# Kernel optimization log

Measured on AMD Instinct MI355X. Metric: run time of the kernel, lower is better.

## Reference

```python
import jax, jax.numpy as jnp
import numpy as np

DIM, NHEADS = 1024, 16
HD = DIM // NHEADS
ROPE_BASE = 10000.0


def rope_cos_sin(seq_len, hd):
    inv_freq = 1.0 / (ROPE_BASE ** (jnp.arange(0, hd, 2, dtype=jnp.float32) / hd))
    t = jnp.arange(seq_len, dtype=jnp.float32)
    freqs = jnp.outer(t, inv_freq)              # [N, hd/2]
    emb = jnp.concatenate([freqs, freqs], -1)   # [N, hd]
    return jnp.cos(emb), jnp.sin(emb)


def rotate_half(x):
    h = x.shape[-1] // 2
    return jnp.concatenate([-x[..., h:], x[..., :h]], -1)


def setup_inputs() -> dict:
    key = jax.random.key(0)
    ks = jax.random.split(key, 5)
    B, N = 1, 2048
    x = jax.random.normal(ks[0], (B, N, DIM), jnp.float32)
    wq = jax.random.normal(ks[1], (DIM, DIM), jnp.float32) * 0.02
    wk = jax.random.normal(ks[2], (DIM, DIM), jnp.float32) * 0.02
    wv = jax.random.normal(ks[3], (DIM, DIM), jnp.float32) * 0.02
    wp = jax.random.normal(ks[4], (DIM, DIM), jnp.float32) * 0.02
    return {"x": x, "wq": wq, "wk": wk, "wv": wv, "wp": wp}


def reference(x, wq, wk, wv, wp):
    B, N, D = x.shape
    H, hd = NHEADS, HD
    # nn.Linear: y = x @ W.T (weights stored [out, in])
    q = (x @ wq.T).reshape(B, N, H, hd)
    k = (x @ wk.T).reshape(B, N, H, hd)
    v = (x @ wv.T).reshape(B, N, H, hd)
    cos, sin = rope_cos_sin(N, hd)
    cos = cos[None, :, None, :]
    sin = sin[None, :, None, :]
    q = q * cos + rotate_half(q) * sin
    k = k * cos + rotate_half(k) * sin
    # SDPA (no mask, non-causal, eval -> no dropout)
    scale = 1.0 / jnp.sqrt(jnp.float32(hd))
    logits = jnp.einsum("bqhd,bkhd->bhqk", q, k) * scale
    attn = jax.nn.softmax(logits, axis=-1)
    out = jnp.einsum("bhqk,bkhd->bqhd", attn, v).reshape(B, N, D)
    return out @ wp.T
```

## Files before the change

### kernel.cpp

```cpp
#include <hip/hip_runtime.h>

typedef short s16x8 __attribute__((ext_vector_type(8)));
typedef float f32x4 __attribute__((ext_vector_type(4)));

__device__ __forceinline__ unsigned short f2bf(float f) {
    unsigned int u = __float_as_uint(f);
    u += 0x7fff + ((u >> 16) & 1);
    return (unsigned short)(u >> 16);
}
__device__ __forceinline__ float bf2f(unsigned short h) {
    return __uint_as_float(((unsigned int)h) << 16);
}
__device__ __forceinline__ f32x4 mfma16(s16x8 a, s16x8 b, f32x4 c) {
    return __builtin_amdgcn_mfma_f32_16x16x32_bf16(a, b, c, 0, 0, 0);
}
__device__ __forceinline__ void async16(const void* g, void* l) {
    __builtin_amdgcn_global_load_lds(
        (const __attribute__((address_space(1))) void*)g,
        (__attribute__((address_space(3))) void*)l, 16, 0, 0);
}

__global__ __launch_bounds__(256) void convert_all(
    const float* __restrict__ x,  const float* __restrict__ wq,
    const float* __restrict__ wk, const float* __restrict__ wv,
    const float* __restrict__ wp,
    unsigned short* __restrict__ xb, unsigned short* __restrict__ wqkvb,
    unsigned short* __restrict__ wpb)
{
    const size_t XN = 2048u * 1024u, WN = 1024u * 1024u;
    size_t e = ((size_t)blockIdx.x * 256 + threadIdx.x) * 4;
    const float* s; unsigned short* d;
    if (e < XN)                { s = x  + e;               d = xb    + e; }
    else if (e < XN + WN)      { s = wq + (e - XN);        d = wqkvb + (e - XN); }
    else if (e < XN + 2 * WN)  { s = wk + (e - XN - WN);   d = wqkvb + (e - XN); }
    else if (e < XN + 3 * WN)  { s = wv + (e - XN - 2*WN); d = wqkvb + (e - XN); }
    else                       { s = wp + (e - XN - 3*WN); d = wpb   + (e - XN - 3*WN); }
    float4 v = *(const float4*)s;
    ushort4 o;
    o.x = f2bf(v.x); o.y = f2bf(v.y); o.z = f2bf(v.z); o.w = f2bf(v.w);
    *(ushort4*)d = o;
}

template<int BN, int C32>
__global__ __launch_bounds__(256) void gemm_mfma(
    const unsigned short* __restrict__ A,
    const unsigned short* __restrict__ B,
    void* __restrict__ C, int Ntot)
{
    __shared__ unsigned short As[128 * 64];
    __shared__ unsigned short Bs[BN * 64];

    const int tid  = threadIdx.x;
    const int wave = tid >> 6, lane = tid & 63;
    const int l16  = lane & 15, quad = lane >> 4;
    const int m0   = blockIdx.y * 128, n0 = blockIdx.x * BN;
    const int wm   = (wave & 1) * 64, wn = (wave >> 1) * (BN / 2);
    constexpr int NT = BN / 32;

    const int srow = lane >> 3;
    const int scol = (lane & 7) * 8;

    f32x4 acc[4][NT] = {};

    for (int k0 = 0; k0 < 1024; k0 += 64) {
        #pragma unroll
        for (int i = 0; i < 4; i++) {
            int j = wave * 4 + i;
            async16(A + (size_t)(m0 + j * 8 + srow) * 1024 + k0 + scol, &As[j * 512]);
        }
        #pragma unroll
        for (int i = 0; i < BN / 32; i++) {
            int j = wave * (BN / 32) + i;
            async16(B + (size_t)(n0 + j * 8 + srow) * 1024 + k0 + scol, &Bs[j * 512]);
        }
        __syncthreads();

        #pragma unroll
        for (int ks = 0; ks < 2; ks++) {
            s16x8 af[4], bfr[NT];
            #pragma unroll
            for (int mt = 0; mt < 4; mt++)
                af[mt] = *(const s16x8*)&As[(wm + mt * 16 + l16) * 64 + ks * 32 + quad * 8];
            #pragma unroll
            for (int nt = 0; nt < NT; nt++)
                bfr[nt] = *(const s16x8*)&Bs[(wn + nt * 16 + l16) * 64 + ks * 32 + quad * 8];
            #pragma unroll
            for (int mt = 0; mt < 4; mt++)
                #pragma unroll
                for (int nt = 0; nt < NT; nt++)
                    acc[mt][nt] = mfma16(af[mt], bfr[nt], acc[mt][nt]);
        }
        __syncthreads();
    }

    #pragma unroll
    for (int mt = 0; mt < 4; mt++)
        #pragma unroll
        for (int nt = 0; nt < NT; nt++)
            #pragma unroll
            for (int r = 0; r < 4; r++) {
                int m = m0 + wm + mt * 16 + quad * 4 + r;
                int n = n0 + wn + nt * 16 + l16;
                size_t idx = (size_t)m * Ntot + n;
                if (C32) ((float*)C)[idx] = acc[mt][nt][r];
                else     ((unsigned short*)C)[idx] = f2bf(acc[mt][nt][r]);
            }
}

__global__ __launch_bounds__(256) void rope_kernel(unsigned short* __restrict__ qkv)
{
    int idx = blockIdx.x * 256 + threadIdx.x;
    int i = idx & 31;
    int h = (idx >> 5) & 15;
    int n = idx >> 9;
    float ang = (float)n * exp2f((float)i * (-13.287712379549449f / 32.0f));
    float c, s;
    sincosf(ang, &c, &s);
    size_t base = (size_t)n * 3072 + h * 64 + i;
    float a0 = bf2f(qkv[base]), a1 = bf2f(qkv[base + 32]);
    qkv[base]      = f2bf(a0 * c + a1 * s);
    qkv[base + 32] = f2bf(a1 * c - a0 * s);
    float b0 = bf2f(qkv[base + 1024]), b1 = bf2f(qkv[base + 1056]);
    qkv[base + 1024] = f2bf(b0 * c + b1 * s);
    qkv[base + 1056] = f2bf(b1 * c - b0 * s);
}

__global__ __launch_bounds__(256) void attn_kernel(
    const unsigned short* __restrict__ qkv,
    unsigned short* __restrict__ O)
{
    const int h  = blockIdx.y;
    const int q0 = blockIdx.x * 64;
    const int tid  = threadIdx.x;
    const int wave = tid >> 6, lane = tid & 63;
    const int l16  = lane & 15, quad = lane >> 4;

    __shared__ unsigned short Ks[128][72];
    __shared__ unsigned short Vt[64][136];
    __shared__ unsigned short Ps[4][16][136];

    const int mq = q0 + wave * 16 + l16;
    const unsigned short* qp = qkv + (size_t)mq * 3072 + h * 64 + quad * 8;
    s16x8 qa0 = *(const s16x8*)qp;
    s16x8 qa1 = *(const s16x8*)(qp + 32);

    f32x4 o[4] = {};
    float lrow[4] = {0.f, 0.f, 0.f, 0.f};

    const int skey = tid >> 1;
    const int sd   = (tid & 1) * 32;

    for (int kt = 0; kt < 2048; kt += 128) {
        {
            const unsigned short* gk = qkv + (size_t)(kt + skey) * 3072 + 1024 + h * 64 + sd;
            const uint4* gk4 = (const uint4*)gk;
            uint4 k0 = gk4[0], k1 = gk4[1], k2 = gk4[2], k3 = gk4[3];
            *(uint4*)&Ks[skey][sd]      = k0;
            *(uint4*)&Ks[skey][sd + 8]  = k1;
            *(uint4*)&Ks[skey][sd + 16] = k2;
            *(uint4*)&Ks[skey][sd + 24] = k3;
            const uint4* gv4 = (const uint4*)(gk + 1024);
            uint4 v0 = gv4[0], v1 = gv4[1], v2 = gv4[2], v3 = gv4[3];
            unsigned short tmp[32];
            *(uint4*)&tmp[0]  = v0; *(uint4*)&tmp[8]  = v1;
            *(uint4*)&tmp[16] = v2; *(uint4*)&tmp[24] = v3;
            #pragma unroll
            for (int j = 0; j < 32; j++)
                Vt[sd + j][skey] = tmp[j];
        }
        __syncthreads();

        f32x4 s[8];
        #pragma unroll
        for (int nt = 0; nt < 8; nt++) {
            s16x8 b0 = *(const s16x8*)&Ks[nt * 16 + l16][quad * 8];
            s16x8 b1 = *(const s16x8*)&Ks[nt * 16 + l16][32 + quad * 8];
            f32x4 z = {};
            z = mfma16(qa0, b0, z);
            z = mfma16(qa1, b1, z);
            s[nt] = z;
        }
        #pragma unroll
        for (int nt = 0; nt < 8; nt++)
            #pragma unroll
            for (int r = 0; r < 4; r++) {
                float p = __expf(s[nt][r] * 0.125f);
                lrow[r] += p;
                Ps[wave][quad * 4 + r][nt * 16 + l16] = f2bf(p);
            }

        s16x8 pa[4];
        #pragma unroll
        for (int kc = 0; kc < 4; kc++)
            pa[kc] = *(const s16x8*)&Ps[wave][l16][kc * 32 + quad * 8];

        #pragma unroll
        for (int dt = 0; dt < 4; dt++)
            #pragma unroll
            for (int kc = 0; kc < 4; kc++) {
                s16x8 vb = *(const s16x8*)&Vt[dt * 16 + l16][kc * 32 + quad * 8];
                o[dt] = mfma16(pa[kc], vb, o[dt]);
            }
        __syncthreads();
    }

    #pragma unroll
    for (int r = 0; r < 4; r++) {
        float v = lrow[r];
        #pragma unroll
        for (int off = 8; off >= 1; off >>= 1)
            v += __shfl_xor(v, off, 64);
        lrow[r] = v;
    }
    #pragma unroll
    for (int r = 0; r < 4; r++) {
        float inv = 1.0f / lrow[r];
        int m = q0 + wave * 16 + quad * 4 + r;
        #pragma unroll
        for (int dt = 0; dt < 4; dt++)
            O[(size_t)m * 1024 + h * 64 + dt * 16 + l16] = f2bf(o[dt][r] * inv);
    }
}

extern "C" void kernel_launch(void* const* d_in, const int* in_sizes, int n_in,
                              void* d_out, int out_size, void* d_ws, size_t ws_size,
                              hipStream_t stream)
{
    const float* x  = (const float*)d_in[0];
    const float* wq = (const float*)d_in[1];
    const float* wk = (const float*)d_in[2];
    const float* wv = (const float*)d_in[3];
    const float* wp = (const float*)d_in[4];

    unsigned short* xb    = (unsigned short*)d_ws;
    unsigned short* wqkvb = xb    + 2u * 1024 * 1024;
    unsigned short* wpb   = wqkvb + 3u * 1024 * 1024;
    unsigned short* qkv   = wpb   + 1u * 1024 * 1024;
    unsigned short* ab    = qkv   + 2048u * 3072;

    convert_all<<<6144, 256, 0, stream>>>(x, wq, wk, wv, wp, xb, wqkvb, wpb);
    gemm_mfma<128, 0><<<dim3(24, 16), 256, 0, stream>>>(xb, wqkvb, qkv, 3072);
    rope_kernel<<<(2048 * 512) / 256, 256, 0, stream>>>(qkv);
    attn_kernel<<<dim3(32, 16), 256, 0, stream>>>(qkv, ab);
    gemm_mfma<64, 1><<<dim3(16, 16), 256, 0, stream>>>(ab, wpb, d_out, 1024);
}
```

Baseline: 177.3 us.

## Split attention over key halves with combine kernel, shrink GEMM tiles for more blocks

Attention is split along the key dimension into two partial passes (grid z=2) that write unnormalized fp32 outputs and row sums, followed by a combine kernel that sums and normalizes into bf16. This doubles the attention grid to fill more CUs on the device. The softmax has no running max, so the partials can be added directly. The V transpose into LDS now writes ushort4 vectors instead of scalar stores, and both GEMMs use smaller tiles (128x64 and 64x64) to launch more blocks. The cost is extra fp32 partial traffic and one more kernel launch.

```diff
diff --git a/kernel.cpp b/kernel.cpp
--- a/kernel.cpp
+++ b/kernel.cpp
@@ -41,51 +41,51 @@
     *(ushort4*)d = o;
 }
 
-template<int BN, int C32>
+template<int BM, int BN, int C32>
 __global__ __launch_bounds__(256) void gemm_mfma(
     const unsigned short* __restrict__ A,
     const unsigned short* __restrict__ B,
     void* __restrict__ C, int Ntot)
 {
-    __shared__ unsigned short As[128 * 64];
+    constexpr int MT = BM / 32, NT = BN / 32;
+    __shared__ unsigned short As[BM * 64];
     __shared__ unsigned short Bs[BN * 64];
 
     const int tid  = threadIdx.x;
     const int wave = tid >> 6, lane = tid & 63;
     const int l16  = lane & 15, quad = lane >> 4;
-    const int m0   = blockIdx.y * 128, n0 = blockIdx.x * BN;
-    const int wm   = (wave & 1) * 64, wn = (wave >> 1) * (BN / 2);
-    constexpr int NT = BN / 32;
+    const int m0   = blockIdx.y * BM, n0 = blockIdx.x * BN;
+    const int wm   = (wave & 1) * (BM / 2), wn = (wave >> 1) * (BN / 2);
 
     const int srow = lane >> 3;
     const int scol = (lane & 7) * 8;
 
-    f32x4 acc[4][NT] = {};
+    f32x4 acc[MT][NT] = {};
 
     for (int k0 = 0; k0 < 1024; k0 += 64) {
         #pragma unroll
-        for (int i = 0; i < 4; i++) {
-            int j = wave * 4 + i;
+        for (int i = 0; i < MT; i++) {
+            int j = wave * MT + i;
             async16(A + (size_t)(m0 + j * 8 + srow) * 1024 + k0 + scol, &As[j * 512]);
         }
         #pragma unroll
-        for (int i = 0; i < BN / 32; i++) {
-            int j = wave * (BN / 32) + i;
+        for (int i = 0; i < NT; i++) {
+            int j = wave * NT + i;
             async16(B + (size_t)(n0 + j * 8 + srow) * 1024 + k0 + scol, &Bs[j * 512]);
         }
         __syncthreads();
 
         #pragma unroll
         for (int ks = 0; ks < 2; ks++) {
-            s16x8 af[4], bfr[NT];
-            #pragma unroll
-            for (int mt = 0; mt < 4; mt++)
+            s16x8 af[MT], bfr[NT];
+            #pragma unroll
+            for (int mt = 0; mt < MT; mt++)
                 af[mt] = *(const s16x8*)&As[(wm + mt * 16 + l16) * 64 + ks * 32 + quad * 8];
             #pragma unroll
             for (int nt = 0; nt < NT; nt++)
                 bfr[nt] = *(const s16x8*)&Bs[(wn + nt * 16 + l16) * 64 + ks * 32 + quad * 8];
             #pragma unroll
-            for (int mt = 0; mt < 4; mt++)
+            for (int mt = 0; mt < MT; mt++)
                 #pragma unroll
                 for (int nt = 0; nt < NT; nt++)
                     acc[mt][nt] = mfma16(af[mt], bfr[nt], acc[mt][nt]);
@@ -94,7 +94,7 @@
     }
 
     #pragma unroll
-    for (int mt = 0; mt < 4; mt++)
+    for (int mt = 0; mt < MT; mt++)
         #pragma unroll
         for (int nt = 0; nt < NT; nt++)
             #pragma unroll
@@ -125,12 +125,13 @@
     qkv[base + 1056] = f2bf(b1 * c - b0 * s);
 }
 
-__global__ __launch_bounds__(256) void attn_kernel(
+__global__ __launch_bounds__(256) void attn_part(
     const unsigned short* __restrict__ qkv,
-    unsigned short* __restrict__ O)
+    float* __restrict__ Opart, float* __restrict__ Lpart)
 {
     const int h  = blockIdx.y;
     const int q0 = blockIdx.x * 64;
+    const int ks = blockIdx.z;
     const int tid  = threadIdx.x;
     const int wave = tid >> 6, lane = tid & 63;
     const int l16  = lane & 15, quad = lane >> 4;
@@ -149,8 +150,11 @@
 
     const int skey = tid >> 1;
     const int sd   = (tid & 1) * 32;
-
-    for (int kt = 0; kt < 2048; kt += 128) {
+    const int vg   = tid & 31;
+    const int vdo  = (tid >> 5) * 8;
+
+    for (int t8 = 0; t8 < 8; t8++) {
+        const int kt = ks * 1024 + t8 * 128;
         {
             const unsigned short* gk = qkv + (size_t)(kt + skey) * 3072 + 1024 + h * 64 + sd;
             const uint4* gk4 = (const uint4*)gk;
@@ -159,14 +163,20 @@
             *(uint4*)&Ks[skey][sd + 8]  = k1;
             *(uint4*)&Ks[skey][sd + 16] = k2;
             *(uint4*)&Ks[skey][sd + 24] = k3;
-            const uint4* gv4 = (const uint4*)(gk + 1024);
-            uint4 v0 = gv4[0], v1 = gv4[1], v2 = gv4[2], v3 = gv4[3];
-            unsigned short tmp[32];
-            *(uint4*)&tmp[0]  = v0; *(uint4*)&tmp[8]  = v1;
-            *(uint4*)&tmp[16] = v2; *(uint4*)&tmp[24] = v3;
-            #pragma unroll
-            for (int j = 0; j < 32; j++)
-                Vt[sd + j][skey] = tmp[j];
+        }
+        {
+            const unsigned short* gv = qkv + (size_t)(kt + 4 * vg) * 3072 + 2048 + h * 64 + vdo;
+            unsigned short a0[8], a1[8], a2[8], a3[8];
+            *(uint4*)a0 = *(const uint4*)gv;
+            *(uint4*)a1 = *(const uint4*)(gv + 3072);
+            *(uint4*)a2 = *(const uint4*)(gv + 2 * 3072);
+            *(uint4*)a3 = *(const uint4*)(gv + 3 * 3072);
+            #pragma unroll
+            for (int d = 0; d < 8; d++) {
+                ushort4 w;
+                w.x = a0[d]; w.y = a1[d]; w.z = a2[d]; w.w = a3[d];
+                *(ushort4*)&Vt[vdo + d][4 * vg] = w;
+            }
         }
         __syncthreads();
 
@@ -214,12 +224,33 @@
     }
     #pragma unroll
     for (int r = 0; r < 4; r++) {
-        float inv = 1.0f / lrow[r];
         int m = q0 + wave * 16 + quad * 4 + r;
+        float* op = Opart + ((size_t)ks * 2048 + m) * 1024 + h * 64;
         #pragma unroll
         for (int dt = 0; dt < 4; dt++)
-            O[(size_t)m * 1024 + h * 64 + dt * 16 + l16] = f2bf(o[dt][r] * inv);
-    }
+            op[dt * 16 + l16] = o[dt][r];
+        if (l16 == 0)
+            Lpart[((size_t)ks * 2048 + m) * 16 + h] = lrow[r];
+    }
+}
+
+__global__ __launch_bounds__(256) void combine(
+    const float* __restrict__ Opart, const float* __restrict__ Lpart,
+    unsigned short* __restrict__ ab)
+{
+    size_t e = ((size_t)blockIdx.x * 256 + threadIdx.x) * 4;
+    int tok = (int)(e >> 10);
+    int h = (int)((e & 1023) >> 6);
+    float l = Lpart[(size_t)tok * 16 + h] + Lpart[(size_t)(2048 + tok) * 16 + h];
+    float inv = 1.0f / l;
+    float4 n0 = *(const float4*)(Opart + e);
+    float4 n1 = *(const float4*)(Opart + (size_t)2048 * 1024 + e);
+    ushort4 w;
+    w.x = f2bf((n0.x + n1.x) * inv);
+    w.y = f2bf((n0.y + n1.y) * inv);
+    w.z = f2bf((n0.z + n1.z) * inv);
+    w.w = f2bf((n0.w + n1.w) * inv);
+    *(ushort4*)(ab + e) = w;
 }
 
 extern "C" void kernel_launch(void* const* d_in, const int* in_sizes, int n_in,
@@ -237,10 +268,13 @@
     unsigned short* wpb   = wqkvb + 3u * 1024 * 1024;
     unsigned short* qkv   = wpb   + 1u * 1024 * 1024;
     unsigned short* ab    = qkv   + 2048u * 3072;
+    float* Opart = (float*)(ab + 2u * 1024 * 1024);
+    float* Lpart = Opart + 2u * 2048 * 1024;
 
     convert_all<<<6144, 256, 0, stream>>>(x, wq, wk, wv, wp, xb, wqkvb, wpb);
-    gemm_mfma<128, 0><<<dim3(24, 16), 256, 0, stream>>>(xb, wqkvb, qkv, 3072);
+    gemm_mfma<128, 64, 0><<<dim3(48, 16), 256, 0, stream>>>(xb, wqkvb, qkv, 3072);
     rope_kernel<<<(2048 * 512) / 256, 256, 0, stream>>>(qkv);
-    attn_kernel<<<dim3(32, 16), 256, 0, stream>>>(qkv, ab);
-    gemm_mfma<64, 1><<<dim3(16, 16), 256, 0, stream>>>(ab, wpb, d_out, 1024);
-}
+    attn_part<<<dim3(32, 16, 2), 256, 0, stream>>>(qkv, Opart, Lpart);
+    combine<<<2048, 256, 0, stream>>>(Opart, Lpart, ab);
+    gemm_mfma<64, 64, 1><<<dim3(16, 32), 256, 0, stream>>>(ab, wpb, d_out, 1024);
+}
```

Measured after the change: 176.6 us. Within noise of the previous version (-0.4%).
